# Performance work log

Measured on AMD Instinct MI355X. Metric: run time of the kernel, lower is better.

The kernel has to match this reference:

```python
import jax, jax.numpy as jnp
import numpy as np

N = 150000   # nodes
E = 600000   # directed edges (before self-loops)
H = 4        # heads
HID = 64     # hidden channels per head
G = 4096     # graphs in batch
IN = 9       # input node features
EPS = 1e-5
NEG_SLOPE = 0.2


def setup_inputs() -> dict:
    key = jax.random.key(0)
    ks = jax.random.split(key, 24)
    x = jax.random.normal(ks[0], (N, IN), jnp.float32)
    edge_index = jax.random.randint(ks[1], (2, E), 0, N, dtype=jnp.int32)
    batch = jnp.sort(jax.random.randint(ks[2], (N,), 0, G)).astype(jnp.int64)
    s = 0.1  # weight scale for numerical sanity
    return {
        "x": x,
        "edge_index": edge_index,
        "batch": batch,
        "gat0_W": jax.random.normal(ks[3], (IN, H * HID), jnp.float32) * s,
        "gat0_asrc": jax.random.normal(ks[4], (H, HID), jnp.float32) * s,
        "gat0_adst": jax.random.normal(ks[5], (H, HID), jnp.float32) * s,
        "gat0_b": jnp.zeros((HID,), jnp.float32),
        "bn0_gamma": jax.random.uniform(ks[6], (HID,), jnp.float32, 0.5, 1.5),
        "bn0_beta": jax.random.normal(ks[7], (HID,), jnp.float32) * s,
        "bn0_mean": jax.random.normal(ks[8], (HID,), jnp.float32) * s,
        "bn0_var": jax.random.uniform(ks[9], (HID,), jnp.float32, 0.5, 1.5),
        "gat_W": jax.random.normal(ks[10], (3, HID, H * HID), jnp.float32) * s,
        "gat_asrc": jax.random.normal(ks[11], (3, H, HID), jnp.float32) * s,
        "gat_adst": jax.random.normal(ks[12], (3, H, HID), jnp.float32) * s,
        "gat_b": jnp.zeros((3, HID), jnp.float32),
        "bn_gamma": jax.random.uniform(ks[13], (3, HID), jnp.float32, 0.5, 1.5),
        "bn_beta": jax.random.normal(ks[14], (3, HID), jnp.float32) * s,
        "bn_mean": jax.random.normal(ks[15], (3, HID), jnp.float32) * s,
        "bn_var": jax.random.uniform(ks[16], (3, HID), jnp.float32, 0.5, 1.5),
        "out_W1": jax.random.normal(ks[17], (HID, HID // 2), jnp.float32) * s,
        "out_b1": jnp.zeros((HID // 2,), jnp.float32),
        "out_W2": jax.random.normal(ks[18], (HID // 2, 1), jnp.float32) * s,
        "out_b2": jnp.zeros((1,), jnp.float32),
    }


def _gat_conv(h_in, W, a_src, a_dst, b, src, dst):
    # PyG GATConv, concat=False (mean over heads), add_self_loops=True, eval-mode dropout.
    n = h_in.shape[0]
    h = (h_in @ W).reshape(n, H, HID)                 # [N,H,C]
    e_s = jnp.einsum("nhc,hc->nh", h, a_src)          # [N,H]
    e_d = jnp.einsum("nhc,hc->nh", h, a_dst)          # [N,H]
    alpha = jax.nn.leaky_relu(e_s[src] + e_d[dst], NEG_SLOPE)  # [E',H]
    amax = jax.ops.segment_max(alpha, dst, num_segments=n)      # every node has a self-loop
    ex = jnp.exp(alpha - amax[dst])
    denom = jax.ops.segment_sum(ex, dst, num_segments=n)
    w = ex / denom[dst]                               # [E',H]
    msg = h[src] * w[:, :, None]                      # [E',H,C]
    out = jax.ops.segment_sum(msg, dst, num_segments=n)  # [N,H,C]
    return out.mean(axis=1) + b                       # [N,C]


def _bn_elu(h, gamma, beta, mean, var):
    h = (h - mean) * jax.lax.rsqrt(var + EPS) * gamma + beta
    return jax.nn.elu(h)


def reference(x, edge_index, batch, gat0_W, gat0_asrc, gat0_adst, gat0_b,
              bn0_gamma, bn0_beta, bn0_mean, bn0_var,
              gat_W, gat_asrc, gat_adst, gat_b,
              bn_gamma, bn_beta, bn_mean, bn_var,
              out_W1, out_b1, out_W2, out_b2):
    n = x.shape[0]
    loops = jnp.arange(n, dtype=edge_index.dtype)
    src = jnp.concatenate([edge_index[0], loops])
    dst = jnp.concatenate([edge_index[1], loops])

    h = _gat_conv(x, gat0_W, gat0_asrc, gat0_adst, gat0_b, src, dst)
    h = _bn_elu(h, bn0_gamma, bn0_beta, bn0_mean, bn0_var)
    for i in range(3):
        r = _gat_conv(h, gat_W[i], gat_asrc[i], gat_adst[i], gat_b[i], src, dst)
        r = _bn_elu(r, bn_gamma[i], bn_beta[i], bn_mean[i], bn_var[i])
        h = h + r

    # global mean pool over graphs
    sums = jax.ops.segment_sum(h, batch, num_segments=G)           # [G,C]
    cnts = jax.ops.segment_sum(jnp.ones((n,), h.dtype), batch, num_segments=G)
    pooled = sums / jnp.maximum(cnts, 1.0)[:, None]

    z = jax.nn.elu(pooled @ out_W1 + out_b1)
    return z @ out_W2 + out_b2                                     # [G,1]
```

## Files before the change

kernel.cpp:

```cpp
#include <hip/hip_runtime.h>

#define NN 150000
#define EE 600000
#define HH 4
#define CC 64
#define GG 4096
#define INF 9

typedef __attribute__((ext_vector_type(8))) short bf16x8;
typedef __attribute__((ext_vector_type(4))) float f32x4;

__device__ __forceinline__ float lrelu(float a){ return a > 0.f ? a : 0.2f*a; }
__device__ __forceinline__ float b2f(unsigned short u){ return __uint_as_float((unsigned)u << 16); }
__device__ __forceinline__ unsigned short f2b(float f){
  unsigned u = __float_as_uint(f);
  return (unsigned short)((u + 0x7fff + ((u >> 16) & 1)) >> 16);
}

__global__ __launch_bounds__(256) void k_count(const int* __restrict__ dst, int* __restrict__ deg){
  int e = blockIdx.x*256 + threadIdx.x;
  if (e < EE) atomicAdd(&deg[dst[e]], 1);
}

__global__ __launch_bounds__(256) void k_scan1(const int* __restrict__ deg, int* __restrict__ excl, int* __restrict__ bsum){
  __shared__ int s[256];
  int tid = threadIdx.x, gid = blockIdx.x*256 + tid;
  int v = (gid < NN) ? deg[gid] : 0;
  s[tid] = v; __syncthreads();
  for (int off = 1; off < 256; off <<= 1){
    int t = (tid >= off) ? s[tid-off] : 0; __syncthreads();
    s[tid] += t; __syncthreads();
  }
  if (gid < NN) excl[gid] = s[tid] - v;
  if (tid == 255) bsum[blockIdx.x] = s[255];
}

__global__ __launch_bounds__(1024) void k_scan2(int* __restrict__ bsum, int nb){
  __shared__ int s[1024];
  int tid = threadIdx.x;
  int v = (tid < nb) ? bsum[tid] : 0;
  s[tid] = v; __syncthreads();
  for (int off = 1; off < 1024; off <<= 1){
    int t = (tid >= off) ? s[tid-off] : 0; __syncthreads();
    s[tid] += t; __syncthreads();
  }
  if (tid < nb) bsum[tid] = s[tid] - v;
}

__global__ __launch_bounds__(256) void k_scan3(int* __restrict__ rp, const int* __restrict__ bsum){
  int gid = blockIdx.x*256 + threadIdx.x;
  if (gid < NN) rp[gid] += bsum[blockIdx.x];
  if (gid == 0) rp[NN] = EE;
}

__global__ __launch_bounds__(256) void k_fill(const int* __restrict__ src, const int* __restrict__ dst,
                                              const int* __restrict__ rp, int* __restrict__ fill,
                                              int* __restrict__ col){
  int e = blockIdx.x*256 + threadIdx.x;
  if (e < EE){
    int d = dst[e];
    int pos = rp[d] + atomicAdd(&fill[d], 1);
    col[pos] = src[e];
  }
}

__global__ __launch_bounds__(256) void k_gstart(const int* __restrict__ batch, int* __restrict__ gstart){
  int g = blockIdx.x*256 + threadIdx.x;
  if (g > GG) return;
  int lo = 0, hi = NN;
  while (lo < hi){ int mid = (lo+hi) >> 1; if (batch[mid] < g) lo = mid+1; else hi = mid; }
  gstart[g] = lo;
}

__global__ __launch_bounds__(256) void k_fold(const float* __restrict__ g0W, const float* __restrict__ g0as,
    const float* __restrict__ g0ad, const float* __restrict__ gW, const float* __restrict__ gas,
    const float* __restrict__ gad, float* __restrict__ Wa0, float* __restrict__ Wa,
    float* __restrict__ Wstk0){
  const int OFF1 = 72, OFF2 = OFF1 + 1536, OFF3 = OFF2 + 2304;
  int t = blockIdx.x*256 + threadIdx.x;
  if (t < OFF1){
    int k = t >> 3, j = t & 7, h = j & 3;
    const float* a = (j < 4) ? g0as : g0ad;
    float s = 0.f;
    for (int c = 0; c < 64; c++) s += g0W[k*256 + h*64 + c] * a[h*64 + c];
    Wa0[t] = s;
  } else if (t < OFF2){
    int u = t - OFF1;
    int i = u / 512, r = u % 512, k = r >> 3, j = r & 7, h = j & 3;
    const float* a = ((j < 4) ? gas : gad) + (size_t)i*256;
    float s = 0.f;
    for (int c = 0; c < 64; c++) s += gW[(size_t)i*16384 + k*256 + h*64 + c] * a[h*64 + c];
    Wa[u] = s;
  } else if (t < OFF3){
    int u = t - OFF2;
    int k = u >> 6, j = u & 63;
    int h = k / 9, c = k - h*9;
    Wstk0[u] = 0.25f * g0W[c*256 + h*64 + j];
  }
}

__global__ __launch_bounds__(256) void k_foldB(const float* __restrict__ gW,
    unsigned short* __restrict__ Wfhi, unsigned short* __restrict__ Wflo){
  int t = blockIdx.x*256 + threadIdx.x;
  if (t >= 3*4*8*64) return;
  int l = t & 63, s = (t >> 6) & 7, c = (t >> 9) & 3, i = t >> 11;
  size_t base = (size_t)i*16384 + (size_t)(((c*8 + s)*64 + l))*8;
  #pragma unroll
  for (int b = 0; b < 8; b++){
    int k = s*32 + ((l >> 4) << 3) + b;
    int h = k >> 6, ci = k & 63;
    int j = (c << 4) + (l & 15);
    float v = 0.25f * gW[(size_t)i*16384 + ci*256 + h*64 + j];
    unsigned short hi = f2b(v);
    unsigned short lo = f2b(v - b2f(hi));
    Wfhi[base + b] = hi;
    Wflo[base + b] = lo;
  }
}

__global__ __launch_bounds__(256) void k_logits9(const float* __restrict__ hin, const float* __restrict__ Wa,
                                                 float* __restrict__ lg){
  int idx = blockIdx.x*256 + threadIdx.x;
  int node = idx >> 3, j = idx & 7;
  if (node >= NN) return;
  const float* r = hin + (size_t)node*INF;
  float s = 0.f;
  #pragma unroll
  for (int k = 0; k < INF; k++) s += r[k] * Wa[k*8 + j];
  lg[(size_t)node*8 + j] = s;
}

__global__ __launch_bounds__(256) void k_wgt(const float* __restrict__ lg, const int* __restrict__ rp,
    const int* __restrict__ col, float* __restrict__ w, float* __restrict__ wself){
  int t = blockIdx.x*256 + threadIdx.x;
  if (t >= NN*4) return;
  int n = t >> 2, h = t & 3;
  float edv = lg[(size_t)n*8 + 4 + h];
  int rb = rp[n], re = rp[n+1];
  float s = 0.f;
  for (int p = rb; p < re; p++){
    float e = __expf(lrelu(lg[(size_t)col[p]*8 + h] + edv));
    w[(size_t)p*4 + h] = e;
    s += e;
  }
  float wsf = __expf(lrelu(lg[(size_t)n*8 + h] + edv));
  float inv = 1.f / (s + wsf);
  for (int p = rb; p < re; p++) w[(size_t)p*4 + h] *= inv;
  wself[t] = wsf * inv;
}

__global__ __launch_bounds__(256) void k_agg9(const float* __restrict__ hin, const float* __restrict__ w,
     const float* __restrict__ wself, const int* __restrict__ rp, const int* __restrict__ col,
     float* __restrict__ aggo){
  int node = (blockIdx.x*256 + threadIdx.x) >> 6;
  int lane = threadIdx.x & 63;
  if (node >= NN) return;
  node = __builtin_amdgcn_readfirstlane(node);
  int rb = rp[node], re = rp[node+1];
  float4 ws4 = *(const float4*)(wself + (size_t)node*4);
  float xself = (lane < INF) ? hin[(size_t)node*INF + lane] : 0.f;
  float acc[4] = {ws4.x*xself, ws4.y*xself, ws4.z*xself, ws4.w*xself};

  int last = re - 1;
  for (int e = rb; e < re; e += 8){
    int ec[8], sidx[8]; float4 wv[8]; float xv[8];
    #pragma unroll
    for (int q = 0; q < 8; q++){ int eq = e + q; ec[q] = (eq <= last) ? eq : last; }
    #pragma unroll
    for (int q = 0; q < 8; q++) sidx[q] = col[ec[q]];
    #pragma unroll
    for (int q = 0; q < 8; q++) wv[q] = *(const float4*)(w + (size_t)ec[q]*4);
    #pragma unroll
    for (int q = 0; q < 8; q++)
      xv[q] = (lane < INF) ? hin[(size_t)sidx[q]*INF + lane] : 0.f;
    int n = re - e;
    #pragma unroll
    for (int q = 0; q < 8; q++){
      if (q < n){
        acc[0] += wv[q].x*xv[q]; acc[1] += wv[q].y*xv[q];
        acc[2] += wv[q].z*xv[q]; acc[3] += wv[q].w*xv[q];
      }
    }
  }

  if (lane < INF){
    float* ap = aggo + (size_t)node*36 + lane;
    ap[0] = acc[0]; ap[INF] = acc[1]; ap[2*INF] = acc[2]; ap[3*INF] = acc[3];
  }
}

__global__ __launch_bounds__(256) void k_agg4b(const unsigned short* __restrict__ hb,
     const float* __restrict__ w, const float* __restrict__ wself, const int* __restrict__ rp,
     const int* __restrict__ col, unsigned short* __restrict__ aggb){
  int wv_id = (blockIdx.x*256 + threadIdx.x) >> 6;
  int lane = threadIdx.x & 63;
  int ns = lane >> 4, q = lane & 15;
  int node = wv_id*4 + ns;
  if (node >= NN) return;
  int rb = rp[node], re = rp[node+1];

  float4 ws4 = *(const float4*)(wself + (size_t)node*4);
  ushort4 xu = *(const ushort4*)(hb + (size_t)node*64 + q*4);
  float x0 = b2f(xu.x), x1 = b2f(xu.y), x2 = b2f(xu.z), x3 = b2f(xu.w);
  float acc[4][4];
  #pragma unroll
  for (int h = 0; h < 4; h++){
    float wh = (h==0)?ws4.x:(h==1)?ws4.y:(h==2)?ws4.z:ws4.w;
    acc[h][0] = wh*x0; acc[h][1] = wh*x1; acc[h][2] = wh*x2; acc[h][3] = wh*x3;
  }

  int d = re - rb;
  d = max(d, __shfl_xor(d, 16));
  d = max(d, __shfl_xor(d, 32));

  for (int i = 0; i < d; i += 2){
    int e0 = rb + i, e1 = rb + i + 1;
    bool v0 = e0 < re, v1 = e1 < re;
    if (v0){
      int s0 = col[e0];
      float4 w0 = *(const float4*)(w + (size_t)e0*4);
      ushort4 u0 = *(const ushort4*)(hb + (size_t)s0*64 + q*4);
      float y0 = b2f(u0.x), y1 = b2f(u0.y), y2 = b2f(u0.z), y3 = b2f(u0.w);
      acc[0][0] += w0.x*y0; acc[0][1] += w0.x*y1; acc[0][2] += w0.x*y2; acc[0][3] += w0.x*y3;
      acc[1][0] += w0.y*y0; acc[1][1] += w0.y*y1; acc[1][2] += w0.y*y2; acc[1][3] += w0.y*y3;
      acc[2][0] += w0.z*y0; acc[2][1] += w0.z*y1; acc[2][2] += w0.z*y2; acc[2][3] += w0.z*y3;
      acc[3][0] += w0.w*y0; acc[3][1] += w0.w*y1; acc[3][2] += w0.w*y2; acc[3][3] += w0.w*y3;
    }
    if (v1){
      int s1 = col[e1];
      float4 w1 = *(const float4*)(w + (size_t)e1*4);
      ushort4 u1 = *(const ushort4*)(hb + (size_t)s1*64 + q*4);
      float y0 = b2f(u1.x), y1 = b2f(u1.y), y2 = b2f(u1.z), y3 = b2f(u1.w);
      acc[0][0] += w1.x*y0; acc[0][1] += w1.x*y1; acc[0][2] += w1.x*y2; acc[0][3] += w1.x*y3;
      acc[1][0] += w1.y*y0; acc[1][1] += w1.y*y1; acc[1][2] += w1.y*y2; acc[1][3] += w1.y*y3;
      acc[2][0] += w1.z*y0; acc[2][1] += w1.z*y1; acc[2][2] += w1.z*y2; acc[2][3] += w1.z*y3;
      acc[3][0] += w1.w*y0; acc[3][1] += w1.w*y1; acc[3][2] += w1.w*y2; acc[3][3] += w1.w*y3;
    }
  }

  #pragma unroll
  for (int h = 0; h < 4; h++){
    ushort4 o = { f2b(acc[h][0]), f2b(acc[h][1]), f2b(acc[h][2]), f2b(acc[h][3]) };
    *(ushort4*)(aggb + (size_t)node*256 + h*64 + q*4) = o;
  }
}

__global__ __launch_bounds__(256, 4) void k_gemmB36(const float* __restrict__ agg, const float* __restrict__ Ws,
    const float* __restrict__ bias, const float* __restrict__ gma, const float* __restrict__ bta,
    const float* __restrict__ mea, const float* __restrict__ var,
    float* __restrict__ hout, unsigned short* __restrict__ hbf,
    const float* __restrict__ WaN, float* __restrict__ lg){
  __shared__ float xs[64*68];
  __shared__ float ws[64*68];
  __shared__ float wal[512];
  int t = threadIdx.x;
  int base = blockIdx.x * 64;
  int r = t >> 4, c2 = t & 15;
  for (int i = t; i < 512; i += 256) wal[i] = WaN[i];

  for (int i = t; i < 64*9; i += 256){
    int nd = i / 9, kk = i - nd*9;
    float4 v = {0.f,0.f,0.f,0.f};
    if (base + nd < NN) v = *(const float4*)(agg + (size_t)(base+nd)*36 + kk*4);
    *(float4*)(xs + nd*44 + kk*4) = v;
  }
  for (int i = t; i < 36*16; i += 256){
    int k = i >> 4, c4 = i & 15;
    *(float4*)(ws + k*68 + c4*4) = *(const float4*)(Ws + (size_t)k*64 + c4*4);
  }
  __syncthreads();

  float acc[4][4];
  #pragma unroll
  for (int i = 0; i < 4; i++)
    #pragma unroll
    for (int u = 0; u < 4; u++) acc[i][u] = 0.f;

  #pragma unroll 2
  for (int k4 = 0; k4 < 36; k4 += 4){
    float4 xv[4], wv[4];
    #pragma unroll
    for (int i = 0; i < 4; i++) xv[i] = *(const float4*)(xs + (4*r+i)*44 + k4);
    #pragma unroll
    for (int u = 0; u < 4; u++) wv[u] = *(const float4*)(ws + (k4+u)*68 + 4*c2);
    #pragma unroll
    for (int i = 0; i < 4; i++){
      float xr[4] = {xv[i].x, xv[i].y, xv[i].z, xv[i].w};
      #pragma unroll
      for (int u = 0; u < 4; u++){
        acc[i][0] += xr[u]*wv[u].x; acc[i][1] += xr[u]*wv[u].y;
        acc[i][2] += xr[u]*wv[u].z; acc[i][3] += xr[u]*wv[u].w;
      }
    }
  }

  __syncthreads();
  int cb = 4*c2;
  float4 bi = *(const float4*)(bias + cb);
  float4 gm = *(const float4*)(gma + cb);
  float4 bt = *(const float4*)(bta + cb);
  float4 me = *(const float4*)(mea + cb);
  float4 va = *(const float4*)(var + cb);
  float sc0 = rsqrtf(va.x + 1e-5f)*gm.x, sc1 = rsqrtf(va.y + 1e-5f)*gm.y;
  float sc2 = rsqrtf(va.z + 1e-5f)*gm.z, sc3 = rsqrtf(va.w + 1e-5f)*gm.w;
  #pragma unroll
  for (int i = 0; i < 4; i++){
    int node = base + 4*r + i;
    if (node < NN){
      float o0 = (acc[i][0] + bi.x - me.x)*sc0 + bt.x;
      float o1 = (acc[i][1] + bi.y - me.y)*sc1 + bt.y;
      float o2 = (acc[i][2] + bi.z - me.z)*sc2 + bt.z;
      float o3 = (acc[i][3] + bi.w - me.w)*sc3 + bt.w;
      o0 = o0 > 0.f ? o0 : (__expf(o0) - 1.f);
      o1 = o1 > 0.f ? o1 : (__expf(o1) - 1.f);
      o2 = o2 > 0.f ? o2 : (__expf(o2) - 1.f);
      o3 = o3 > 0.f ? o3 : (__expf(o3) - 1.f);
      float4 st = {o0, o1, o2, o3};
      *(float4*)(hout + (size_t)node*64 + cb) = st;
      uint2 pb = { (unsigned)f2b(o0) | ((unsigned)f2b(o1) << 16),
                   (unsigned)f2b(o2) | ((unsigned)f2b(o3) << 16) };
      *(uint2*)(hbf + (size_t)node*64 + cb) = pb;
      *(float4*)(xs + (4*r+i)*68 + cb) = st;
    }
  }
  __syncthreads();
  int nd = t >> 2, jq = (t & 3) * 2;
  int node = base + nd;
  if (node < NN){
    float s0 = 0.f, s1 = 0.f;
    #pragma unroll 4
    for (int k = 0; k < 64; k += 4){
      float4 xv = *(const float4*)(xs + nd*68 + k);
      const float* w0 = wal + k*8 + jq;
      s0 += xv.x*w0[0] + xv.y*w0[8] + xv.z*w0[16] + xv.w*w0[24];
      s1 += xv.x*w0[1] + xv.y*w0[9] + xv.z*w0[17] + xv.w*w0[25];
    }
    float2 sv = {s0, s1};
    *(float2*)(lg + (size_t)node*8 + jq) = sv;
  }
}

template<bool LOGITS>
__global__ __launch_bounds__(256) void k_gemmBM(const unsigned short* __restrict__ aggb,
    const unsigned short* __restrict__ Wfhi, const unsigned short* __restrict__ Wflo,
    const float* __restrict__ bias, const float* __restrict__ gma, const float* __restrict__ bta,
    const float* __restrict__ mea, const float* __restrict__ var,
    const float* __restrict__ hres, float* __restrict__ hout, unsigned short* __restrict__ hbf,
    const float* __restrict__ WaN, float* __restrict__ lg){
  __shared__ float xs[64*68];
  __shared__ float wal[512];
  int t = threadIdx.x, lane = t & 63, w = t >> 6;
  int base = blockIdx.x * 64;
  if (LOGITS){ for (int i = t; i < 512; i += 256) wal[i] = WaN[i]; }

  int anode = base + (w << 4) + (lane & 15);
  if (anode >= NN) anode = NN - 1;
  const unsigned short* ap = aggb + (size_t)anode*256 + ((lane >> 4) << 3);
  bf16x8 af[8];
  #pragma unroll
  for (int s = 0; s < 8; s++) af[s] = *(const bf16x8*)(ap + s*32);

  f32x4 acch[4], accl[4];
  #pragma unroll
  for (int c = 0; c < 4; c++){ acch[c] = (f32x4)0.f; accl[c] = (f32x4)0.f; }

  #pragma unroll
  for (int s = 0; s < 8; s++){
    #pragma unroll
    for (int c = 0; c < 4; c++){
      int fidx = ((c*8 + s)*64 + lane)*8;
      bf16x8 bh = *(const bf16x8*)(Wfhi + fidx);
      bf16x8 bl = *(const bf16x8*)(Wflo + fidx);
      acch[c] = __builtin_amdgcn_mfma_f32_16x16x32_bf16(af[s], bh, acch[c], 0, 0, 0);
      accl[c] = __builtin_amdgcn_mfma_f32_16x16x32_bf16(af[s], bl, accl[c], 0, 0, 0);
    }
  }

  int rr = (w << 4) + ((lane >> 4) << 2);
  int cc = lane & 15;
  #pragma unroll
  for (int c = 0; c < 4; c++){
    #pragma unroll
    for (int r = 0; r < 4; r++)
      xs[(rr + r)*68 + (c << 4) + cc] = acch[c][r] + accl[c][r];
  }
  __syncthreads();

  for (int i = t; i < 64*64; i += 256){
    int nd = i >> 6, j = i & 63;
    int node = base + nd;
    if (node < NN){
      float o = xs[nd*68 + j] + bias[j];
      o = (o - mea[j]) * rsqrtf(var[j] + 1e-5f) * gma[j] + bta[j];
      o = o > 0.f ? o : (__expf(o) - 1.f);
      o += hres[(size_t)node*64 + j];
      hout[(size_t)node*64 + j] = o;
      if (LOGITS){
        hbf[(size_t)node*64 + j] = f2b(o);
        xs[nd*68 + j] = o;
      }
    }
  }
  if (LOGITS){
    __syncthreads();
    int nd = t >> 2, jq = (t & 3) * 2;
    int node = base + nd;
    if (node < NN){
      float s0 = 0.f, s1 = 0.f;
      #pragma unroll 4
      for (int k = 0; k < 64; k += 4){
        float4 xv = *(const float4*)(xs + nd*68 + k);
        const float* w0 = wal + k*8 + jq;
        s0 += xv.x*w0[0] + xv.y*w0[8] + xv.z*w0[16] + xv.w*w0[24];
        s1 += xv.x*w0[1] + xv.y*w0[9] + xv.z*w0[17] + xv.w*w0[25];
      }
      float2 sv = {s0, s1};
      *(float2*)(lg + (size_t)node*8 + jq) = sv;
    }
  }
}

__global__ __launch_bounds__(64) void k_pool(const float* __restrict__ h, const int* __restrict__ gstart,
                                             float* __restrict__ pooled){
  int g = blockIdx.x; int lane = threadIdx.x;
  int beg = gstart[g], end = gstart[g+1];
  float acc = 0.f;
  for (int n = beg; n < end; n++) acc += h[(size_t)n*64 + lane];
  float cnt = (float)(end - beg);
  pooled[(size_t)g*64 + lane] = acc / fmaxf(cnt, 1.f);
}

__global__ __launch_bounds__(256) void k_mlp(const float* __restrict__ pooled, const float* __restrict__ W1,
                                             const float* __restrict__ b1, const float* __restrict__ W2,
                                             const float* __restrict__ b2, float* __restrict__ out){
  int g = (blockIdx.x*256 + threadIdx.x) >> 6;
  int lane = threadIdx.x & 63;
  if (g >= GG) return;
  float pv = pooled[(size_t)g*64 + lane];
  int j = lane & 31, half = lane >> 5;
  float z = half ? 0.f : b1[j];
  #pragma unroll
  for (int c = 0; c < 32; c++){
    int cc = half*32 + c;
    z += __shfl(pv, cc) * W1[cc*32 + j];
  }
  z += __shfl_xor(z, 32);
  float o = 0.f;
  if (half == 0){
    z = z > 0.f ? z : (__expf(z) - 1.f);
    o = z * W2[j];
  }
  o += __shfl_xor(o, 1); o += __shfl_xor(o, 2); o += __shfl_xor(o, 4);
  o += __shfl_xor(o, 8); o += __shfl_xor(o, 16);
  if (lane == 0) out[g] = o + b2[0];
}

extern "C" void kernel_launch(void* const* d_in, const int* in_sizes, int n_in,
                              void* d_out, int out_size, void* d_ws, size_t ws_size,
                              hipStream_t stream) {
  const float* x    = (const float*)d_in[0];
  const int*   ei   = (const int*)d_in[1];
  const int*   batch= (const int*)d_in[2];
  const float* g0W  = (const float*)d_in[3];
  const float* g0as = (const float*)d_in[4];
  const float* g0ad = (const float*)d_in[5];
  const float* g0b  = (const float*)d_in[6];
  const float* bn0g = (const float*)d_in[7];
  const float* bn0b = (const float*)d_in[8];
  const float* bn0m = (const float*)d_in[9];
  const float* bn0v = (const float*)d_in[10];
  const float* gW   = (const float*)d_in[11];
  const float* gas  = (const float*)d_in[12];
  const float* gad  = (const float*)d_in[13];
  const float* gb   = (const float*)d_in[14];
  const float* bng  = (const float*)d_in[15];
  const float* bnb  = (const float*)d_in[16];
  const float* bnm  = (const float*)d_in[17];
  const float* bnv  = (const float*)d_in[18];
  const float* W1   = (const float*)d_in[19];
  const float* b1   = (const float*)d_in[20];
  const float* W2   = (const float*)d_in[21];
  const float* b2   = (const float*)d_in[22];
  float* out = (float*)d_out;
  (void)in_sizes; (void)n_in; (void)out_size; (void)ws_size;

  char* base = (char*)d_ws; size_t off = 0;
  auto alloc = [&](size_t b)->void*{ void* p = base + off; off = (off + b + 255) & ~(size_t)255; return p; };
  unsigned short* aggb = (unsigned short*)alloc((size_t)NN*256*2);
  float* agg32  = (float*)alloc((size_t)NN*36*4);
  float* h_cur  = (float*)alloc((size_t)NN*64*4);
  unsigned short* hbf = (unsigned short*)alloc((size_t)NN*64*2);
  float* lg     = (float*)alloc((size_t)NN*8*4);
  float* wE     = (float*)alloc((size_t)EE*4*4);
  float* wS     = (float*)alloc((size_t)NN*4*4);
  int*   deg    = (int*)alloc((size_t)NN*4);
  int*   fill   = (int*)alloc((size_t)NN*4);
  int*   rp     = (int*)alloc((size_t)(NN+1)*4);
  int*   col    = (int*)alloc((size_t)EE*4);
  int*   bsum   = (int*)alloc(1024*4);
  int*   gstart = (int*)alloc((size_t)(GG+1)*4);
  float* pooled = (float*)alloc((size_t)GG*64*4);
  float* Wa0    = (float*)alloc((size_t)72*4);
  float* Wa     = (float*)alloc((size_t)1536*4);
  float* Wstk0  = (float*)alloc((size_t)2304*4);
  unsigned short* Wfhi = (unsigned short*)alloc((size_t)3*16384*2);
  unsigned short* Wflo = (unsigned short*)alloc((size_t)3*16384*2);

  const int* esrc = ei;
  const int* edst = ei + EE;

  hipMemsetAsync(deg, 0, (size_t)NN*4, stream);
  hipMemsetAsync(fill, 0, (size_t)NN*4, stream);

  int nb1 = (NN + 255)/256;
  k_count<<<(EE+255)/256, 256, 0, stream>>>(edst, deg);
  k_scan1<<<nb1, 256, 0, stream>>>(deg, rp, bsum);
  k_scan2<<<1, 1024, 0, stream>>>(bsum, nb1);
  k_scan3<<<nb1, 256, 0, stream>>>(rp, bsum);
  k_fill<<<(EE+255)/256, 256, 0, stream>>>(esrc, edst, rp, fill, col);
  k_gstart<<<(GG+256)/256, 256, 0, stream>>>(batch, gstart);
  k_fold<<<16, 256, 0, stream>>>(g0W, g0as, g0ad, gW, gas, gad, Wa0, Wa, Wstk0);
  k_foldB<<<24, 256, 0, stream>>>(gW, Wfhi, Wflo);

  int nlog  = (NN*8 + 255)/256;
  int nwave = NN/4;
  int n4b   = (NN + 15)/16;
  int ngB   = (NN + 63)/64;
  int nnrm  = (NN*4 + 255)/256;

  k_logits9<<<nlog, 256, 0, stream>>>(x, Wa0, lg);
  k_wgt<<<nnrm, 256, 0, stream>>>(lg, rp, col, wE, wS);
  k_agg9<<<nwave, 256, 0, stream>>>(x, wE, wS, rp, col, agg32);
  k_gemmB36<<<ngB, 256, 0, stream>>>(agg32, Wstk0, g0b, bn0g, bn0b, bn0m, bn0v,
                                     h_cur, hbf, Wa, lg);
  for (int i = 0; i < 3; i++){
    k_wgt<<<nnrm, 256, 0, stream>>>(lg, rp, col, wE, wS);
    k_agg4b<<<n4b, 256, 0, stream>>>(hbf, wE, wS, rp, col, aggb);
    if (i < 2)
      k_gemmBM<true><<<ngB, 256, 0, stream>>>(aggb, Wfhi + (size_t)i*16384, Wflo + (size_t)i*16384,
                                              gb + (size_t)i*64,
                                              bng + (size_t)i*64, bnb + (size_t)i*64,
                                              bnm + (size_t)i*64, bnv + (size_t)i*64,
                                              h_cur, h_cur, hbf, Wa + (size_t)(i+1)*512, lg);
    else
      k_gemmBM<false><<<ngB, 256, 0, stream>>>(aggb, Wfhi + (size_t)i*16384, Wflo + (size_t)i*16384,
                                               gb + (size_t)i*64,
                                               bng + (size_t)i*64, bnb + (size_t)i*64,
                                               bnm + (size_t)i*64, bnv + (size_t)i*64,
                                               h_cur, h_cur, hbf, nullptr, nullptr);
  }

  k_pool<<<GG, 64, 0, stream>>>(h_cur, gstart, pooled);
  k_mlp<<<(GG*64 + 255)/256, 256, 0, stream>>>(pooled, W1, b1, W2, b2, out);
}
```

Before: 538.7 us.

## Fuse edge aggregation into MFMA GEMM kernel via LDS tile, ping-pong bf16 features

The separate aggregation kernel is merged into the GEMM/BN/ELU kernel. Each block first aggregates its 64 nodes' weighted neighbor features into a bf16 LDS tile (64x264), then feeds that tile to the MFMA GEMM, reusing the same LDS for the epilogue. This removes the global write and read of the NN x 256 bf16 aggregate buffer and one launch per layer. Because the input features are now read by other blocks while being rewritten, two bf16 feature buffers alternate between layers. The large LDS footprint (about 34KB) may limit occupancy for the latency-bound gather phase.

```diff
diff --git a/kernel.cpp b/kernel.cpp
--- a/kernel.cpp
+++ b/kernel.cpp
@@ -189,62 +189,6 @@
   }
 }
 
-__global__ __launch_bounds__(256) void k_agg4b(const unsigned short* __restrict__ hb,
-     const float* __restrict__ w, const float* __restrict__ wself, const int* __restrict__ rp,
-     const int* __restrict__ col, unsigned short* __restrict__ aggb){
-  int wv_id = (blockIdx.x*256 + threadIdx.x) >> 6;
-  int lane = threadIdx.x & 63;
-  int ns = lane >> 4, q = lane & 15;
-  int node = wv_id*4 + ns;
-  if (node >= NN) return;
-  int rb = rp[node], re = rp[node+1];
-
-  float4 ws4 = *(const float4*)(wself + (size_t)node*4);
-  ushort4 xu = *(const ushort4*)(hb + (size_t)node*64 + q*4);
-  float x0 = b2f(xu.x), x1 = b2f(xu.y), x2 = b2f(xu.z), x3 = b2f(xu.w);
-  float acc[4][4];
-  #pragma unroll
-  for (int h = 0; h < 4; h++){
-    float wh = (h==0)?ws4.x:(h==1)?ws4.y:(h==2)?ws4.z:ws4.w;
-    acc[h][0] = wh*x0; acc[h][1] = wh*x1; acc[h][2] = wh*x2; acc[h][3] = wh*x3;
-  }
-
-  int d = re - rb;
-  d = max(d, __shfl_xor(d, 16));
-  d = max(d, __shfl_xor(d, 32));
-
-  for (int i = 0; i < d; i += 2){
-    int e0 = rb + i, e1 = rb + i + 1;
-    bool v0 = e0 < re, v1 = e1 < re;
-    if (v0){
-      int s0 = col[e0];
-      float4 w0 = *(const float4*)(w + (size_t)e0*4);
-      ushort4 u0 = *(const ushort4*)(hb + (size_t)s0*64 + q*4);
-      float y0 = b2f(u0.x), y1 = b2f(u0.y), y2 = b2f(u0.z), y3 = b2f(u0.w);
-      acc[0][0] += w0.x*y0; acc[0][1] += w0.x*y1; acc[0][2] += w0.x*y2; acc[0][3] += w0.x*y3;
-      acc[1][0] += w0.y*y0; acc[1][1] += w0.y*y1; acc[1][2] += w0.y*y2; acc[1][3] += w0.y*y3;
-      acc[2][0] += w0.z*y0; acc[2][1] += w0.z*y1; acc[2][2] += w0.z*y2; acc[2][3] += w0.z*y3;
-      acc[3][0] += w0.w*y0; acc[3][1] += w0.w*y1; acc[3][2] += w0.w*y2; acc[3][3] += w0.w*y3;
-    }
-    if (v1){
-      int s1 = col[e1];
-      float4 w1 = *(const float4*)(w + (size_t)e1*4);
-      ushort4 u1 = *(const ushort4*)(hb + (size_t)s1*64 + q*4);
-      float y0 = b2f(u1.x), y1 = b2f(u1.y), y2 = b2f(u1.z), y3 = b2f(u1.w);
-      acc[0][0] += w1.x*y0; acc[0][1] += w1.x*y1; acc[0][2] += w1.x*y2; acc[0][3] += w1.x*y3;
-      acc[1][0] += w1.y*y0; acc[1][1] += w1.y*y1; acc[1][2] += w1.y*y2; acc[1][3] += w1.y*y3;
-      acc[2][0] += w1.z*y0; acc[2][1] += w1.z*y1; acc[2][2] += w1.z*y2; acc[2][3] += w1.z*y3;
-      acc[3][0] += w1.w*y0; acc[3][1] += w1.w*y1; acc[3][2] += w1.w*y2; acc[3][3] += w1.w*y3;
-    }
-  }
-
-  #pragma unroll
-  for (int h = 0; h < 4; h++){
-    ushort4 o = { f2b(acc[h][0]), f2b(acc[h][1]), f2b(acc[h][2]), f2b(acc[h][3]) };
-    *(ushort4*)(aggb + (size_t)node*256 + h*64 + q*4) = o;
-  }
-}
-
 __global__ __launch_bounds__(256, 4) void k_gemmB36(const float* __restrict__ agg, const float* __restrict__ Ws,
     const float* __restrict__ bias, const float* __restrict__ gma, const float* __restrict__ bta,
     const float* __restrict__ mea, const float* __restrict__ var,
@@ -341,21 +285,80 @@
 }
 
 template<bool LOGITS>
-__global__ __launch_bounds__(256) void k_gemmBM(const unsigned short* __restrict__ aggb,
+__global__ __launch_bounds__(256, 4) void k_fuse(const unsigned short* __restrict__ hbin,
+    const float* __restrict__ w, const float* __restrict__ wself,
+    const int* __restrict__ rp, const int* __restrict__ col,
     const unsigned short* __restrict__ Wfhi, const unsigned short* __restrict__ Wflo,
     const float* __restrict__ bias, const float* __restrict__ gma, const float* __restrict__ bta,
     const float* __restrict__ mea, const float* __restrict__ var,
-    const float* __restrict__ hres, float* __restrict__ hout, unsigned short* __restrict__ hbf,
+    const float* __restrict__ hres, float* __restrict__ hout, unsigned short* __restrict__ hbout,
     const float* __restrict__ WaN, float* __restrict__ lg){
-  __shared__ float xs[64*68];
+  __shared__ unsigned short al[64*264];
   __shared__ float wal[512];
-  int t = threadIdx.x, lane = t & 63, w = t >> 6;
+  int t = threadIdx.x, lane = t & 63, wv = t >> 6;
   int base = blockIdx.x * 64;
   if (LOGITS){ for (int i = t; i < 512; i += 256) wal[i] = WaN[i]; }
 
-  int anode = base + (w << 4) + (lane & 15);
-  if (anode >= NN) anode = NN - 1;
-  const unsigned short* ap = aggb + (size_t)anode*256 + ((lane >> 4) << 3);
+  {
+    int ns = lane >> 4, q = lane & 15;
+    for (int p = 0; p < 4; p++){
+      int nd = wv*16 + p*4 + ns;
+      int node = base + nd;
+      unsigned short* arow = al + (size_t)nd*264;
+      int rb = 0, re = 0;
+      if (node < NN){ rb = rp[node]; re = rp[node+1]; }
+      int d = re - rb;
+      d = max(d, __shfl_xor(d, 16));
+      d = max(d, __shfl_xor(d, 32));
+      float acc[4][4];
+      {
+        float4 ws4 = {0.f,0.f,0.f,0.f};
+        float x0=0.f, x1=0.f, x2=0.f, x3=0.f;
+        if (node < NN){
+          ws4 = *(const float4*)(wself + (size_t)node*4);
+          ushort4 xu = *(const ushort4*)(hbin + (size_t)node*64 + q*4);
+          x0 = b2f(xu.x); x1 = b2f(xu.y); x2 = b2f(xu.z); x3 = b2f(xu.w);
+        }
+        #pragma unroll
+        for (int h = 0; h < 4; h++){
+          float wh = (h==0)?ws4.x:(h==1)?ws4.y:(h==2)?ws4.z:ws4.w;
+          acc[h][0] = wh*x0; acc[h][1] = wh*x1; acc[h][2] = wh*x2; acc[h][3] = wh*x3;
+        }
+      }
+      for (int i2 = 0; i2 < d; i2 += 2){
+        int e0 = rb + i2, e1 = rb + i2 + 1;
+        if (e0 < re){
+          int s0 = col[e0];
+          float4 w0 = *(const float4*)(w + (size_t)e0*4);
+          ushort4 u0 = *(const ushort4*)(hbin + (size_t)s0*64 + q*4);
+          float y0=b2f(u0.x), y1=b2f(u0.y), y2=b2f(u0.z), y3=b2f(u0.w);
+          acc[0][0]+=w0.x*y0; acc[0][1]+=w0.x*y1; acc[0][2]+=w0.x*y2; acc[0][3]+=w0.x*y3;
+          acc[1][0]+=w0.y*y0; acc[1][1]+=w0.y*y1; acc[1][2]+=w0.y*y2; acc[1][3]+=w0.y*y3;
+          acc[2][0]+=w0.z*y0; acc[2][1]+=w0.z*y1; acc[2][2]+=w0.z*y2; acc[2][3]+=w0.z*y3;
+          acc[3][0]+=w0.w*y0; acc[3][1]+=w0.w*y1; acc[3][2]+=w0.w*y2; acc[3][3]+=w0.w*y3;
+        }
+        if (e1 < re){
+          int s1 = col[e1];
+          float4 w1 = *(const float4*)(w + (size_t)e1*4);
+          ushort4 u1 = *(const ushort4*)(hbin + (size_t)s1*64 + q*4);
+          float y0=b2f(u1.x), y1=b2f(u1.y), y2=b2f(u1.z), y3=b2f(u1.w);
+          acc[0][0]+=w1.x*y0; acc[0][1]+=w1.x*y1; acc[0][2]+=w1.x*y2; acc[0][3]+=w1.x*y3;
+          acc[1][0]+=w1.y*y0; acc[1][1]+=w1.y*y1; acc[1][2]+=w1.y*y2; acc[1][3]+=w1.y*y3;
+          acc[2][0]+=w1.z*y0; acc[2][1]+=w1.z*y1; acc[2][2]+=w1.z*y2; acc[2][3]+=w1.z*y3;
+          acc[3][0]+=w1.w*y0; acc[3][1]+=w1.w*y1; acc[3][2]+=w1.w*y2; acc[3][3]+=w1.w*y3;
+        }
+      }
+      #pragma unroll
+      for (int h = 0; h < 4; h++){
+        ushort4 o = { f2b(acc[h][0]), f2b(acc[h][1]), f2b(acc[h][2]), f2b(acc[h][3]) };
+        *(ushort4*)(arow + h*64 + q*4) = o;
+      }
+    }
+  }
+  __syncthreads();
+
+  int arow_i = wv*16 + (lane & 15);
+  const unsigned short* ap = al + (size_t)arow_i*264 + ((lane >> 4) << 3);
   bf16x8 af[8];
   #pragma unroll
   for (int s = 0; s < 8; s++) af[s] = *(const bf16x8*)(ap + s*32);
@@ -376,40 +379,46 @@
     }
   }
 
-  int rr = (w << 4) + ((lane >> 4) << 2);
-  int cc = lane & 15;
-  #pragma unroll
-  for (int c = 0; c < 4; c++){
-    #pragma unroll
-    for (int r = 0; r < 4; r++)
-      xs[(rr + r)*68 + (c << 4) + cc] = acch[c][r] + accl[c][r];
+  float* df = (float*)(al + (size_t)wv*16*264);
+  {
+    int rr = ((lane >> 4) << 2), cc = lane & 15;
+    #pragma unroll
+    for (int c = 0; c < 4; c++)
+      #pragma unroll
+      for (int r = 0; r < 4; r++)
+        df[(rr + r)*68 + (c << 4) + cc] = acch[c][r] + accl[c][r];
   }
   __syncthreads();
 
-  for (int i = t; i < 64*64; i += 256){
-    int nd = i >> 6, j = i & 63;
-    int node = base + nd;
-    if (node < NN){
-      float o = xs[nd*68 + j] + bias[j];
-      o = (o - mea[j]) * rsqrtf(var[j] + 1e-5f) * gma[j] + bta[j];
-      o = o > 0.f ? o : (__expf(o) - 1.f);
-      o += hres[(size_t)node*64 + j];
-      hout[(size_t)node*64 + j] = o;
-      if (LOGITS){
-        hbf[(size_t)node*64 + j] = f2b(o);
-        xs[nd*68 + j] = o;
+  {
+    int j = lane;
+    float bi = bias[j], bt2 = bta[j], me = mea[j];
+    float sc = rsqrtf(var[j] + 1e-5f) * gma[j];
+    #pragma unroll 4
+    for (int it = 0; it < 16; it++){
+      int node = base + wv*16 + it;
+      if (node < NN){
+        float o = df[it*68 + j] + bi;
+        o = (o - me)*sc + bt2;
+        o = o > 0.f ? o : (__expf(o) - 1.f);
+        o += hres[(size_t)node*64 + j];
+        hout[(size_t)node*64 + j] = o;
+        if (LOGITS){
+          hbout[(size_t)node*64 + j] = f2b(o);
+          df[it*68 + j] = o;
+        }
       }
     }
   }
   if (LOGITS){
     __syncthreads();
-    int nd = t >> 2, jq = (t & 3) * 2;
-    int node = base + nd;
+    int nd = lane >> 2, jq = (lane & 3) * 2;
+    int node = base + wv*16 + nd;
     if (node < NN){
       float s0 = 0.f, s1 = 0.f;
       #pragma unroll 4
       for (int k = 0; k < 64; k += 4){
-        float4 xv = *(const float4*)(xs + nd*68 + k);
+        float4 xv = *(const float4*)(df + nd*68 + k);
         const float* w0 = wal + k*8 + jq;
         s0 += xv.x*w0[0] + xv.y*w0[8] + xv.z*w0[16] + xv.w*w0[24];
         s1 += xv.x*w0[1] + xv.y*w0[9] + xv.z*w0[17] + xv.w*w0[25];
@@ -486,10 +495,10 @@
 
   char* base = (char*)d_ws; size_t off = 0;
   auto alloc = [&](size_t b)->void*{ void* p = base + off; off = (off + b + 255) & ~(size_t)255; return p; };
-  unsigned short* aggb = (unsigned short*)alloc((size_t)NN*256*2);
   float* agg32  = (float*)alloc((size_t)NN*36*4);
   float* h_cur  = (float*)alloc((size_t)NN*64*4);
-  unsigned short* hbf = (unsigned short*)alloc((size_t)NN*64*2);
+  unsigned short* hbfA = (unsigned short*)alloc((size_t)NN*64*2);
+  unsigned short* hbfB = (unsigned short*)alloc((size_t)NN*64*2);
   float* lg     = (float*)alloc((size_t)NN*8*4);
   float* wE     = (float*)alloc((size_t)EE*4*4);
   float* wS     = (float*)alloc((size_t)NN*4*4);
@@ -524,7 +533,6 @@
 
   int nlog  = (NN*8 + 255)/256;
   int nwave = NN/4;
-  int n4b   = (NN + 15)/16;
   int ngB   = (NN + 63)/64;
   int nnrm  = (NN*4 + 255)/256;
 
@@ -532,22 +540,25 @@
   k_wgt<<<nnrm, 256, 0, stream>>>(lg, rp, col, wE, wS);
   k_agg9<<<nwave, 256, 0, stream>>>(x, wE, wS, rp, col, agg32);
   k_gemmB36<<<ngB, 256, 0, stream>>>(agg32, Wstk0, g0b, bn0g, bn0b, bn0m, bn0v,
-                                     h_cur, hbf, Wa, lg);
+                                     h_cur, hbfA, Wa, lg);
   for (int i = 0; i < 3; i++){
+    const unsigned short* hin = (i & 1) ? hbfB : hbfA;
+    unsigned short* hbo       = (i & 1) ? hbfA : hbfB;
     k_wgt<<<nnrm, 256, 0, stream>>>(lg, rp, col, wE, wS);
-    k_agg4b<<<n4b, 256, 0, stream>>>(hbf, wE, wS, rp, col, aggb);
     if (i < 2)
-      k_gemmBM<true><<<ngB, 256, 0, stream>>>(aggb, Wfhi + (size_t)i*16384, Wflo + (size_t)i*16384,
-                                              gb + (size_t)i*64,
-                                              bng + (size_t)i*64, bnb + (size_t)i*64,
-                                              bnm + (size_t)i*64, bnv + (size_t)i*64,
-                                              h_cur, h_cur, hbf, Wa + (size_t)(i+1)*512, lg);
+      k_fuse<true><<<ngB, 256, 0, stream>>>(hin, wE, wS, rp, col,
+                                            Wfhi + (size_t)i*16384, Wflo + (size_t)i*16384,
+                                            gb + (size_t)i*64,
+                                            bng + (size_t)i*64, bnb + (size_t)i*64,
+                                            bnm + (size_t)i*64, bnv + (size_t)i*64,
+                                            h_cur, h_cur, hbo, Wa + (size_t)(i+1)*512, lg);
     else
-      k_gemmBM<false><<<ngB, 256, 0, stream>>>(aggb, Wfhi + (size_t)i*16384, Wflo + (size_t)i*16384,
-                                               gb + (size_t)i*64,
-                                               bng + (size_t)i*64, bnb + (size_t)i*64,
-                                               bnm + (size_t)i*64, bnv + (size_t)i*64,
-                                               h_cur, h_cur, hbf, nullptr, nullptr);
+      k_fuse<false><<<ngB, 256, 0, stream>>>(hin, wE, wS, rp, col,
+                                             Wfhi + (size_t)i*16384, Wflo + (size_t)i*16384,
+                                             gb + (size_t)i*64,
+                                             bng + (size_t)i*64, bnb + (size_t)i*64,
+                                             bnm + (size_t)i*64, bnv + (size_t)i*64,
+                                             h_cur, h_cur, nullptr, nullptr, nullptr);
   }
 
   k_pool<<<GG, 64, 0, stream>>>(h_cur, gstart, pooled);
```

Result: slower. 596.0 us (+10.6%).

## Stage folded GEMM weights in LDS and double node tile per block

Applied to the files above, without the earlier changes.

The residual GAT GEMM kernel now copies both the high and low bf16 weight fragments (64 KB) into shared memory once per block. Blocks grow to 512 threads covering 128 nodes, so eight waves share one copy instead of each wave streaming the weights from global memory. The epilogue is reorganised so each wave handles its own 16 rows with the batch-norm scale and shift precomputed per column, reusing the weight buffer as the output staging tile. The cost is a 64 KB+ LDS footprint per block, which limits blocks per CU, plus an up-front weight copy and an extra barrier before the MFMA loop.

```diff
diff --git a/kernel.cpp b/kernel.cpp
--- a/kernel.cpp
+++ b/kernel.cpp
@@ -341,25 +341,38 @@
 }
 
 template<bool LOGITS>
-__global__ __launch_bounds__(256) void k_gemmBM(const unsigned short* __restrict__ aggb,
+__global__ __launch_bounds__(512, 4) void k_gemmBM(const unsigned short* __restrict__ aggb,
     const unsigned short* __restrict__ Wfhi, const unsigned short* __restrict__ Wflo,
     const float* __restrict__ bias, const float* __restrict__ gma, const float* __restrict__ bta,
     const float* __restrict__ mea, const float* __restrict__ var,
     const float* __restrict__ hres, float* __restrict__ hout, unsigned short* __restrict__ hbf,
     const float* __restrict__ WaN, float* __restrict__ lg){
-  __shared__ float xs[64*68];
+  __shared__ unsigned short wbuf[32768];
   __shared__ float wal[512];
-  int t = threadIdx.x, lane = t & 63, w = t >> 6;
-  int base = blockIdx.x * 64;
-  if (LOGITS){ for (int i = t; i < 512; i += 256) wal[i] = WaN[i]; }
-
-  int anode = base + (w << 4) + (lane & 15);
+  int t = threadIdx.x, lane = t & 63, wv = t >> 6;
+  int base = blockIdx.x * 128;
+  if (LOGITS){ for (int i = t; i < 512; i += 512) wal[i] = WaN[i];
+               if (t < 512) wal[t] = WaN[t]; }
+
+  {
+    uint4* wb = (uint4*)wbuf;
+    const uint4* gh = (const uint4*)Wfhi;
+    const uint4* gl = (const uint4*)Wflo;
+    #pragma unroll
+    for (int i = 0; i < 4; i++) wb[t + i*512] = gh[t + i*512];
+    #pragma unroll
+    for (int i = 0; i < 4; i++) wb[2048 + t + i*512] = gl[t + i*512];
+  }
+
+  int anode = base + (wv << 4) + (lane & 15);
   if (anode >= NN) anode = NN - 1;
   const unsigned short* ap = aggb + (size_t)anode*256 + ((lane >> 4) << 3);
   bf16x8 af[8];
   #pragma unroll
   for (int s = 0; s < 8; s++) af[s] = *(const bf16x8*)(ap + s*32);
 
+  __syncthreads();
+
   f32x4 acch[4], accl[4];
   #pragma unroll
   for (int c = 0; c < 4; c++){ acch[c] = (f32x4)0.f; accl[c] = (f32x4)0.f; }
@@ -369,35 +382,44 @@
     #pragma unroll
     for (int c = 0; c < 4; c++){
       int fidx = ((c*8 + s)*64 + lane)*8;
-      bf16x8 bh = *(const bf16x8*)(Wfhi + fidx);
-      bf16x8 bl = *(const bf16x8*)(Wflo + fidx);
+      bf16x8 bh = *(const bf16x8*)(wbuf + fidx);
+      bf16x8 bl = *(const bf16x8*)(wbuf + 16384 + fidx);
       acch[c] = __builtin_amdgcn_mfma_f32_16x16x32_bf16(af[s], bh, acch[c], 0, 0, 0);
       accl[c] = __builtin_amdgcn_mfma_f32_16x16x32_bf16(af[s], bl, accl[c], 0, 0, 0);
     }
   }
-
-  int rr = (w << 4) + ((lane >> 4) << 2);
-  int cc = lane & 15;
-  #pragma unroll
-  for (int c = 0; c < 4; c++){
-    #pragma unroll
-    for (int r = 0; r < 4; r++)
-      xs[(rr + r)*68 + (c << 4) + cc] = acch[c][r] + accl[c][r];
-  }
   __syncthreads();
 
-  for (int i = t; i < 64*64; i += 256){
-    int nd = i >> 6, j = i & 63;
-    int node = base + nd;
-    if (node < NN){
-      float o = xs[nd*68 + j] + bias[j];
-      o = (o - mea[j]) * rsqrtf(var[j] + 1e-5f) * gma[j] + bta[j];
-      o = o > 0.f ? o : (__expf(o) - 1.f);
-      o += hres[(size_t)node*64 + j];
-      hout[(size_t)node*64 + j] = o;
-      if (LOGITS){
-        hbf[(size_t)node*64 + j] = f2b(o);
-        xs[nd*68 + j] = o;
+  float* df = (float*)wbuf;
+  {
+    int rr = (wv << 4) + ((lane >> 4) << 2);
+    int cc = lane & 15;
+    #pragma unroll
+    for (int c = 0; c < 4; c++)
+      #pragma unroll
+      for (int r = 0; r < 4; r++)
+        df[(rr + r)*68 + (c << 4) + cc] = acch[c][r] + accl[c][r];
+  }
+  __syncthreads();
+
+  {
+    int j = lane;
+    float bi = bias[j], bt2 = bta[j], me = mea[j];
+    float sc = rsqrtf(var[j] + 1e-5f) * gma[j];
+    #pragma unroll 4
+    for (int it = 0; it < 16; it++){
+      int nd = (wv << 4) + it;
+      int node = base + nd;
+      if (node < NN){
+        float o = df[nd*68 + j] + bi;
+        o = (o - me)*sc + bt2;
+        o = o > 0.f ? o : (__expf(o) - 1.f);
+        o += hres[(size_t)node*64 + j];
+        hout[(size_t)node*64 + j] = o;
+        if (LOGITS){
+          hbf[(size_t)node*64 + j] = f2b(o);
+          df[nd*68 + j] = o;
+        }
       }
     }
   }
@@ -409,7 +431,7 @@
       float s0 = 0.f, s1 = 0.f;
       #pragma unroll 4
       for (int k = 0; k < 64; k += 4){
-        float4 xv = *(const float4*)(xs + nd*68 + k);
+        float4 xv = *(const float4*)(df + nd*68 + k);
         const float* w0 = wal + k*8 + jq;
         s0 += xv.x*w0[0] + xv.y*w0[8] + xv.z*w0[16] + xv.w*w0[24];
         s1 += xv.x*w0[1] + xv.y*w0[9] + xv.z*w0[17] + xv.w*w0[25];
@@ -526,6 +548,7 @@
   int nwave = NN/4;
   int n4b   = (NN + 15)/16;
   int ngB   = (NN + 63)/64;
+  int ngBM  = (NN + 127)/128;
   int nnrm  = (NN*4 + 255)/256;
 
   k_logits9<<<nlog, 256, 0, stream>>>(x, Wa0, lg);
@@ -537,17 +560,17 @@
     k_wgt<<<nnrm, 256, 0, stream>>>(lg, rp, col, wE, wS);
     k_agg4b<<<n4b, 256, 0, stream>>>(hbf, wE, wS, rp, col, aggb);
     if (i < 2)
-      k_gemmBM<true><<<ngB, 256, 0, stream>>>(aggb, Wfhi + (size_t)i*16384, Wflo + (size_t)i*16384,
-                                              gb + (size_t)i*64,
-                                              bng + (size_t)i*64, bnb + (size_t)i*64,
-                                              bnm + (size_t)i*64, bnv + (size_t)i*64,
-                                              h_cur, h_cur, hbf, Wa + (size_t)(i+1)*512, lg);
-    else
-      k_gemmBM<false><<<ngB, 256, 0, stream>>>(aggb, Wfhi + (size_t)i*16384, Wflo + (size_t)i*16384,
+      k_gemmBM<true><<<ngBM, 512, 0, stream>>>(aggb, Wfhi + (size_t)i*16384, Wflo + (size_t)i*16384,
                                                gb + (size_t)i*64,
                                                bng + (size_t)i*64, bnb + (size_t)i*64,
                                                bnm + (size_t)i*64, bnv + (size_t)i*64,
-                                               h_cur, h_cur, hbf, nullptr, nullptr);
+                                               h_cur, h_cur, hbf, Wa + (size_t)(i+1)*512, lg);
+    else
+      k_gemmBM<false><<<ngBM, 512, 0, stream>>>(aggb, Wfhi + (size_t)i*16384, Wflo + (size_t)i*16384,
+                                                gb + (size_t)i*64,
+                                                bng + (size_t)i*64, bnb + (size_t)i*64,
+                                                bnm + (size_t)i*64, bnv + (size_t)i*64,
+                                                h_cur, h_cur, hbf, nullptr, nullptr);
   }
 
   k_pool<<<GG, 64, 0, stream>>>(h_cur, gstart, pooled);
```

Measured after the change: 514.3 us. 4.5% less time.
